# Optimization experiments

Hardware: AMD Instinct MI355X
Metric: run time of the kernel (lower is better)

Reference implementation:

```python
import jax, jax.numpy as jnp
import numpy as np

N = 100000
E = 1600000
H = 128
G = 64  # num graphs


def setup_inputs() -> dict:
    key = jax.random.key(0)
    ks = jax.random.split(key, 20)
    s = 1.0 / np.sqrt(H)
    inp = {
        'x': jax.random.normal(ks[0], (N,), jnp.float32),
        'edge_index': jax.random.randint(ks[1], (2, E), 0, N, jnp.int32),
        'edge_attr': jax.random.normal(ks[2], (E, 1), jnp.float32),
        'batch': jnp.sort(jax.random.randint(ks[3], (N,), 0, G, jnp.int32)),
        # node/edge encoders (Linear(1, H))
        'ne_w': jax.random.normal(ks[4], (1, H), jnp.float32),
        'ne_b': jnp.zeros((H,), jnp.float32),
        'ee_w': jax.random.normal(ks[5], (1, H), jnp.float32),
        'ee_b': jnp.zeros((H,), jnp.float32),
        # conv1: internal edge lin (Linear(H,H)) + MLP (H->H->H)
        'lin1_w': jax.random.normal(ks[6], (H, H), jnp.float32) * s,
        'lin1_b': jnp.zeros((H,), jnp.float32),
        'w11': jax.random.normal(ks[7], (H, H), jnp.float32) * s,
        'b11': jnp.zeros((H,), jnp.float32),
        'w12': jax.random.normal(ks[8], (H, H), jnp.float32) * s,
        'b12': jnp.zeros((H,), jnp.float32),
        # conv2
        'lin2_w': jax.random.normal(ks[9], (H, H), jnp.float32) * s,
        'lin2_b': jnp.zeros((H,), jnp.float32),
        'w21': jax.random.normal(ks[10], (H, H), jnp.float32) * s,
        'b21': jnp.zeros((H,), jnp.float32),
        'w22': jax.random.normal(ks[11], (H, H), jnp.float32) * s,
        'b22': jnp.zeros((H,), jnp.float32),
    }
    return inp


def _gine(h, edge_index, e, lin_w, lin_b, w1, b1, w2, b2, eps=0.0):
    # message: ReLU(x_j + Lin(edge_attr)), aggregated (sum) at target nodes
    src, dst = edge_index[0], edge_index[1]
    m = jax.nn.relu(h[src] + e @ lin_w + lin_b)           # [E, H]
    agg = jax.ops.segment_sum(m, dst, num_segments=N)      # [N, H]
    z = (1.0 + eps) * h + agg
    return jax.nn.relu(z @ w1 + b1) @ w2 + b2


def reference(x, edge_index, edge_attr, batch, ne_w, ne_b, ee_w, ee_b,
              lin1_w, lin1_b, w11, b11, w12, b12,
              lin2_w, lin2_b, w21, b21, w22, b22):
    h = x.reshape(-1, 1) @ ne_w + ne_b                     # [N, H]
    e = edge_attr @ ee_w + ee_b                            # [E, H]
    h = jax.nn.relu(_gine(h, edge_index, e, lin1_w, lin1_b, w11, b11, w12, b12))
    h = jax.nn.relu(_gine(h, edge_index, e, lin2_w, lin2_b, w21, b21, w22, b22))
    # global mean pool per graph
    sums = jax.ops.segment_sum(h, batch, num_segments=G)   # [G, H]
    cnt = jax.ops.segment_sum(jnp.ones((N,), h.dtype), batch, num_segments=G)
    return sums / jnp.maximum(cnt, 1.0)[:, None]
```

## Files before the change

### kernel.cpp

```cpp
#include <hip/hip_runtime.h>

typedef unsigned short u16;
typedef unsigned int u32;
typedef __bf16 bfrag __attribute__((ext_vector_type(8)));
typedef float f32x4 __attribute__((ext_vector_type(4)));
typedef float f32x2 __attribute__((ext_vector_type(2)));

__device__ __forceinline__ u16 f2bf(float f) {
    u32 u = __float_as_uint(f);
    u32 r = (u + 0x7FFFu + ((u >> 16) & 1u)) >> 16;
    return (u16)r;
}
__device__ __forceinline__ float bf2f(u32 h) {
    return __uint_as_float(h << 16);
}

__global__ __launch_bounds__(256) void prepack_consts_kernel(
    const float* __restrict__ w11, const float* __restrict__ w12,
    const float* __restrict__ w21, const float* __restrict__ w22,
    u16* __restrict__ hi, u16* __restrict__ lo,
    const float* __restrict__ ne_b, const float* __restrict__ ee_w, const float* __restrict__ ee_b,
    const float* __restrict__ lin1_w, const float* __restrict__ lin1_b,
    const float* __restrict__ lin2_w, const float* __restrict__ lin2_b,
    float* __restrict__ u1, float* __restrict__ C1, float* __restrict__ u2, float* __restrict__ C2)
{
    if (blockIdx.x == 256) {
        int c = threadIdx.x;
        if (c < 128) {
            float s1 = 0.f, t1 = 0.f, s2 = 0.f, t2 = 0.f;
            for (int k = 0; k < 128; ++k) {
                float w1 = lin1_w[k * 128 + c];
                float w2 = lin2_w[k * 128 + c];
                float ew = ee_w[k], eb = ee_b[k];
                s1 = fmaf(ew, w1, s1); t1 = fmaf(eb, w1, t1);
                s2 = fmaf(ew, w2, s2); t2 = fmaf(eb, w2, t2);
            }
            u1[c] = s1; C1[c] = t1 + lin1_b[c] + ne_b[c];
            u2[c] = s2; C2[c] = t2 + lin2_b[c];
        }
        return;
    }
    int which = blockIdx.x >> 6;
    const float* w = (which == 0) ? w11 : (which == 1) ? w12 : (which == 2) ? w21 : w22;
    int o = (blockIdx.x & 63) * 256 + threadIdx.x;
    int j = o & 7;
    int lane = (o >> 3) & 63;
    int ct = (o >> 9) & 7;
    int ks = o >> 12;
    int k = ks * 32 + ((lane >> 4) * 8) + j;
    int c = ct * 16 + (lane & 15);
    float v = w[k * 128 + c];
    u16 h = f2bf(v);
    float vh = bf2f(h);
    u16 l = f2bf(v - vh);
    hi[which * 16384 + o] = h;
    lo[which * 16384 + o] = l;
}

__global__ __launch_bounds__(1024) void bcount_kernel(
    const int* __restrict__ dst, int* __restrict__ bcnt, int* __restrict__ done,
    int* __restrict__ bstart, int* __restrict__ bcur, int E, int nb)
{
    __shared__ int h[256];
    __shared__ int is_last;
    if (threadIdx.x < 256) h[threadIdx.x] = 0;
    __syncthreads();
    int idx = blockIdx.x * 1024 + threadIdx.x;
    int e = idx * 4;
    if (e + 3 < E) {
        int4 d4 = ((const int4*)dst)[idx];
        atomicAdd(&h[d4.x >> 9], 1);
        atomicAdd(&h[d4.y >> 9], 1);
        atomicAdd(&h[d4.z >> 9], 1);
        atomicAdd(&h[d4.w >> 9], 1);
    } else {
        for (int k = e; k < E; ++k) atomicAdd(&h[dst[k] >> 9], 1);
    }
    __syncthreads();
    if (threadIdx.x < 256 && h[threadIdx.x]) atomicAdd(&bcnt[threadIdx.x], h[threadIdx.x]);
    __syncthreads();
    if (threadIdx.x == 0) {
        __threadfence();
        is_last = (atomicAdd(done, 1) == (int)gridDim.x - 1);
    }
    __syncthreads();
    if (!is_last) return;
    if (threadIdx.x < 256) h[threadIdx.x] = atomicAdd(&bcnt[threadIdx.x], 0);
    __syncthreads();
    __shared__ int excl[256];
    if (threadIdx.x < 64) {
        int l = threadIdx.x;
        int v0 = h[4 * l], v1 = h[4 * l + 1], v2 = h[4 * l + 2], v3 = h[4 * l + 3];
        int tot = v0 + v1 + v2 + v3;
        int run = tot;
#pragma unroll
        for (int off = 1; off < 64; off <<= 1) {
            int t = __shfl_up(run, off);
            if (l >= off) run += t;
        }
        int ex = run - tot;
        excl[4 * l] = ex;
        excl[4 * l + 1] = ex + v0;
        excl[4 * l + 2] = ex + v0 + v1;
        excl[4 * l + 3] = ex + v0 + v1 + v2;
    }
    __syncthreads();
    if (threadIdx.x < nb) {
        int ex = excl[threadIdx.x];
        bstart[threadIdx.x] = ex;
        bcur[threadIdx.x] = ex;
        if (threadIdx.x == nb - 1) bstart[nb] = ex + h[threadIdx.x];
    }
}

__global__ __launch_bounds__(1024) void bin_kernel(
    const int* __restrict__ src, const int* __restrict__ dst, const float* __restrict__ eattr,
    int* __restrict__ bucket_cursor,
    int2* __restrict__ binned, int E, int nb)
{
    __shared__ int hist[256];
    __shared__ int basel[256];
    __shared__ int gbase[256];
    __shared__ int2 stage[4096];
    __shared__ unsigned char sb[4096];
    const int tid = threadIdx.x;
    const int e0 = blockIdx.x * 4096;
    const int valid = min(4096, E - e0);

    if (tid < 256) hist[tid] = 0;
    __syncthreads();

    int d[4], s[4], a[4], rk[4];
    bool ok[4];
    const int eb = e0 + tid * 4;
    if (eb + 3 < E) {
        int4 d4 = *(const int4*)(dst + eb);
        int4 s4 = *(const int4*)(src + eb);
        int4 a4 = *(const int4*)((const int*)eattr + eb);
        d[0] = d4.x; d[1] = d4.y; d[2] = d4.z; d[3] = d4.w;
        s[0] = s4.x; s[1] = s4.y; s[2] = s4.z; s[3] = s4.w;
        a[0] = a4.x; a[1] = a4.y; a[2] = a4.z; a[3] = a4.w;
        ok[0] = ok[1] = ok[2] = ok[3] = true;
    } else {
#pragma unroll
        for (int k = 0; k < 4; ++k) {
            int e = eb + k;
            ok[k] = e < E;
            if (ok[k]) {
                d[k] = dst[e];
                s[k] = src[e];
                a[k] = __float_as_int(eattr[e]);
            }
        }
    }
#pragma unroll
    for (int k = 0; k < 4; ++k) {
        if (ok[k]) rk[k] = atomicAdd(&hist[d[k] >> 9], 1);
    }
    __syncthreads();
    if (tid < 64) {
        int l = tid;
        int v0 = hist[4 * l], v1 = hist[4 * l + 1], v2 = hist[4 * l + 2], v3 = hist[4 * l + 3];
        int tot = v0 + v1 + v2 + v3;
        int run = tot;
#pragma unroll
        for (int off = 1; off < 64; off <<= 1) {
            int t = __shfl_up(run, off);
            if (l >= off) run += t;
        }
        int ex = run - tot;
        basel[4 * l] = ex;
        basel[4 * l + 1] = ex + v0;
        basel[4 * l + 2] = ex + v0 + v1;
        basel[4 * l + 3] = ex + v0 + v1 + v2;
    }
    __syncthreads();
    if (tid < nb && hist[tid] > 0) gbase[tid] = atomicAdd(&bucket_cursor[tid], hist[tid]);
#pragma unroll
    for (int k = 0; k < 4; ++k) {
        if (ok[k]) {
            int b = d[k] >> 9;
            int pos = basel[b] + rk[k];
            stage[pos] = make_int2(s[k] | ((d[k] & 511) << 17), a[k]);
            sb[pos] = (unsigned char)b;
        }
    }
    __syncthreads();
    for (int i = tid; i < valid; i += 1024) {
        int b = (int)sb[i];
        binned[gbase[b] + (i - basel[b])] = stage[i];
    }
}

__global__ __launch_bounds__(1024) void fine_kernel(
    const int2* __restrict__ binned, const int* __restrict__ bstart,
    int* __restrict__ rowptr, int2* __restrict__ edges, int N, int nbuckets)
{
    __shared__ int hist[512];
    __shared__ int excl[512];
    const int tid = threadIdx.x;
    const int b = blockIdx.x;
    const int s0 = bstart[b], s1 = bstart[b + 1];
    if (tid < 512) hist[tid] = 0;
    __syncthreads();
    for (int i = s0 + tid; i < s1; i += 1024)
        atomicAdd(&hist[(binned[i].x >> 17) & 511], 1);
    __syncthreads();
    if (tid < 64) {
        int l = tid;
        int v[8], pre[8];
        int tot = 0;
#pragma unroll
        for (int k = 0; k < 8; ++k) { v[k] = hist[8 * l + k]; pre[k] = tot; tot += v[k]; }
        int run = tot;
#pragma unroll
        for (int off = 1; off < 64; off <<= 1) {
            int t = __shfl_up(run, off);
            if (l >= off) run += t;
        }
        int ex = run - tot;
#pragma unroll
        for (int k = 0; k < 8; ++k) excl[8 * l + k] = ex + pre[k];
    }
    __syncthreads();
    const int nbase = b << 9;
    if (tid < 512 && nbase + tid < N) rowptr[nbase + tid] = s0 + excl[tid];
    if (b == nbuckets - 1 && tid == 0) rowptr[N] = s1;
    __syncthreads();
    for (int i = s0 + tid; i < s1; i += 1024) {
        int2 ed = binned[i];
        int dlo = (ed.x >> 17) & 511;
        ed.x &= 0x1FFFF;
        int pos = atomicAdd(&excl[dlo], 1);
        edges[s0 + pos] = ed;
    }
}


__global__ __launch_bounds__(256) void pull1_kernel(
    const float* __restrict__ x,
    const int* __restrict__ rowptr, const int2* __restrict__ edges,
    const float* __restrict__ ne_w, const float* __restrict__ ne_b,
    const float* __restrict__ u1, const float* __restrict__ C1,
    u16* __restrict__ zb, int N)
{
    int lane = threadIdx.x & 63;
    int node = blockIdx.x * 4 + (threadIdx.x >> 6);
    if (node >= N) return;
    f32x2 A  = *(const f32x2*)(ne_w + 2 * lane);
    f32x2 Bv = *(const f32x2*)(u1   + 2 * lane);
    f32x2 Cv = *(const f32x2*)(C1   + 2 * lane);
    f32x2 nb = *(const f32x2*)(ne_b + 2 * lane);
    const f32x2 zero = {0.f, 0.f};
    int jb = rowptr[node], je = rowptr[node + 1];
    f32x2 acc = zero;
    int j = jb;
    for (; j + 8 <= je; j += 8) {
        float xs[8], av[8];
#pragma unroll
        for (int t = 0; t < 8; ++t) {
            int2 ep = edges[j + t];
            int s = __builtin_amdgcn_readfirstlane(ep.x);
            av[t] = __int_as_float(__builtin_amdgcn_readfirstlane(ep.y));
            xs[t] = x[s];
        }
#pragma unroll
        for (int t = 0; t < 8; ++t) {
            f32x2 m = __builtin_elementwise_fma((f32x2){xs[t], xs[t]}, A,
                        __builtin_elementwise_fma((f32x2){av[t], av[t]}, Bv, Cv));
            acc += __builtin_elementwise_max(m, zero);
        }
    }
    for (; j < je; ++j) {
        int2 ep = edges[j];
        int s = __builtin_amdgcn_readfirstlane(ep.x);
        float av = __int_as_float(__builtin_amdgcn_readfirstlane(ep.y));
        float xs = x[s];
        f32x2 m = __builtin_elementwise_fma((f32x2){xs, xs}, A,
                    __builtin_elementwise_fma((f32x2){av, av}, Bv, Cv));
        acc += __builtin_elementwise_max(m, zero);
    }
    float xn = x[node];
    f32x2 z = __builtin_elementwise_fma((f32x2){xn, xn}, A, nb) + acc;
    ((u32*)(zb + (long)node * 128))[lane] = (u32)f2bf(z.x) | ((u32)f2bf(z.y) << 16);
}

__global__ __launch_bounds__(256) void pull2_kernel(
    const u16* __restrict__ h1b,
    const int* __restrict__ rowptr, const int2* __restrict__ edges,
    const float* __restrict__ u2, const float* __restrict__ C2,
    u16* __restrict__ zb2, int N)
{
    int lane = threadIdx.x & 63;
    int node = blockIdx.x * 4 + (threadIdx.x >> 6);
    if (node >= N) return;
    f32x2 Bv = *(const f32x2*)(u2 + 2 * lane);
    f32x2 Cv = *(const f32x2*)(C2 + 2 * lane);
    const f32x2 zero = {0.f, 0.f};
    int jb = rowptr[node], je = rowptr[node + 1];
    f32x2 acc = zero;
    int j = jb;
    for (; j + 8 <= je; j += 8) {
        int sidx[8];
        float av[8];
        u32 hv[8];
#pragma unroll
        for (int t = 0; t < 8; ++t) {
            int2 ep = edges[j + t];
            sidx[t] = __builtin_amdgcn_readfirstlane(ep.x);
            av[t] = __int_as_float(__builtin_amdgcn_readfirstlane(ep.y));
        }
#pragma unroll
        for (int t = 0; t < 8; ++t)
            hv[t] = *(const u32*)(h1b + (long)sidx[t] * 128 + 2 * lane);
#pragma unroll
        for (int t = 0; t < 8; ++t) {
            f32x2 h = { __uint_as_float(hv[t] << 16), __uint_as_float(hv[t] & 0xFFFF0000u) };
            f32x2 m = h + __builtin_elementwise_fma((f32x2){av[t], av[t]}, Bv, Cv);
            acc += __builtin_elementwise_max(m, zero);
        }
    }
    for (; j < je; ++j) {
        int2 ep = edges[j];
        int s = __builtin_amdgcn_readfirstlane(ep.x);
        float av = __int_as_float(__builtin_amdgcn_readfirstlane(ep.y));
        u32 hv = *(const u32*)(h1b + (long)s * 128 + 2 * lane);
        f32x2 h = { __uint_as_float(hv << 16), __uint_as_float(hv & 0xFFFF0000u) };
        f32x2 m = h + __builtin_elementwise_fma((f32x2){av, av}, Bv, Cv);
        acc += __builtin_elementwise_max(m, zero);
    }
    u32 hn = *(const u32*)(h1b + (long)node * 128 + 2 * lane);
    f32x2 hnv = { __uint_as_float(hn << 16), __uint_as_float(hn & 0xFFFF0000u) };
    f32x2 z = hnv + acc;
    ((u32*)(zb2 + (long)node * 128))[lane] = (u32)f2bf(z.x) | ((u32)f2bf(z.y) << 16);
}

__global__ __launch_bounds__(256) void mlp_kernel(
    const u16* __restrict__ zb,
    const u16* __restrict__ w1hi, const u16* __restrict__ w1lo,
    const u16* __restrict__ w2hi, const u16* __restrict__ w2lo,
    const float* __restrict__ b1, const float* __restrict__ b2,
    u16* __restrict__ outb)
{
    __shared__ __align__(16) u16 tls[64][136];
    const int lane = threadIdx.x & 63;
    const int wv = threadIdx.x >> 6;
    const int m = lane & 15;
    const int q = lane >> 4;
    const int ko = q * 8;
    const long tile_row = (long)blockIdx.x * 64 + wv * 16;

    f32x4 acc[8];
#pragma unroll
    for (int ct = 0; ct < 8; ++ct) acc[ct] = (f32x4){0.f, 0.f, 0.f, 0.f};

#pragma unroll
    for (int ks = 0; ks < 4; ++ks) {
        bfrag a = *(const bfrag*)(zb + (tile_row + m) * 128 + ks * 32 + ko);
#pragma unroll
        for (int ct = 0; ct < 8; ++ct) {
            const int off = (((ks * 8 + ct) * 64) + lane) * 8;
            bfrag bh = *(const bfrag*)(w1hi + off);
            bfrag bl = *(const bfrag*)(w1lo + off);
            acc[ct] = __builtin_amdgcn_mfma_f32_16x16x32_bf16(a, bh, acc[ct], 0, 0, 0);
            acc[ct] = __builtin_amdgcn_mfma_f32_16x16x32_bf16(a, bl, acc[ct], 0, 0, 0);
        }
    }
#pragma unroll
    for (int ct = 0; ct < 8; ++ct) {
        float bv = b1[ct * 16 + m];
#pragma unroll
        for (int r = 0; r < 4; ++r) {
            float v = fmaxf(acc[ct][r] + bv, 0.f);
            tls[wv * 16 + q * 4 + r][ct * 16 + m] = f2bf(v);
        }
    }
    __syncthreads();

    f32x4 acc2[8];
#pragma unroll
    for (int ct = 0; ct < 8; ++ct) acc2[ct] = (f32x4){0.f, 0.f, 0.f, 0.f};

#pragma unroll
    for (int ks = 0; ks < 4; ++ks) {
        bfrag a = *(const bfrag*)(&tls[wv * 16 + m][ks * 32 + ko]);
#pragma unroll
        for (int ct = 0; ct < 8; ++ct) {
            const int off = (((ks * 8 + ct) * 64) + lane) * 8;
            bfrag bh = *(const bfrag*)(w2hi + off);
            bfrag bl = *(const bfrag*)(w2lo + off);
            acc2[ct] = __builtin_amdgcn_mfma_f32_16x16x32_bf16(a, bh, acc2[ct], 0, 0, 0);
            acc2[ct] = __builtin_amdgcn_mfma_f32_16x16x32_bf16(a, bl, acc2[ct], 0, 0, 0);
        }
    }
    __syncthreads();
#pragma unroll
    for (int ct = 0; ct < 8; ++ct) {
        float bv = b2[ct * 16 + m];
#pragma unroll
        for (int r = 0; r < 4; ++r) {
            float v = fmaxf(acc2[ct][r] + bv, 0.f);
            tls[wv * 16 + q * 4 + r][ct * 16 + m] = f2bf(v);
        }
    }
    __syncthreads();
    const long base_row = (long)blockIdx.x * 64;
#pragma unroll
    for (int it = 0; it < 4; ++it) {
        int chunk = threadIdx.x + it * 256;
        int row = chunk >> 4;
        int c8 = (chunk & 15) * 8;
        *(uint4*)(outb + (base_row + row) * 128 + c8) = *(const uint4*)(&tls[row][c8]);
    }
}

__global__ __launch_bounds__(256) void mlp_pool_kernel(
    const u16* __restrict__ zb,
    const u16* __restrict__ w1hi, const u16* __restrict__ w1lo,
    const u16* __restrict__ w2hi, const u16* __restrict__ w2lo,
    const float* __restrict__ b1, const float* __restrict__ b2,
    const int* __restrict__ batch, float* __restrict__ poolacc, int N)
{
    __shared__ __align__(16) u16 tls[64][136];
    __shared__ int bsh[64];
    const int lane = threadIdx.x & 63;
    const int wv = threadIdx.x >> 6;
    const int m = lane & 15;
    const int q = lane >> 4;
    const int ko = q * 8;
    const long tile_row = (long)blockIdx.x * 64 + wv * 16;
    const long base_row = (long)blockIdx.x * 64;

    if (threadIdx.x < 64) {
        long node = base_row + threadIdx.x;
        bsh[threadIdx.x] = (node < N) ? batch[node] : -1;
    }

    f32x4 acc[8];
#pragma unroll
    for (int ct = 0; ct < 8; ++ct) acc[ct] = (f32x4){0.f, 0.f, 0.f, 0.f};

#pragma unroll
    for (int ks = 0; ks < 4; ++ks) {
        bfrag a = *(const bfrag*)(zb + (tile_row + m) * 128 + ks * 32 + ko);
#pragma unroll
        for (int ct = 0; ct < 8; ++ct) {
            const int off = (((ks * 8 + ct) * 64) + lane) * 8;
            bfrag bh = *(const bfrag*)(w1hi + off);
            bfrag bl = *(const bfrag*)(w1lo + off);
            acc[ct] = __builtin_amdgcn_mfma_f32_16x16x32_bf16(a, bh, acc[ct], 0, 0, 0);
            acc[ct] = __builtin_amdgcn_mfma_f32_16x16x32_bf16(a, bl, acc[ct], 0, 0, 0);
        }
    }
#pragma unroll
    for (int ct = 0; ct < 8; ++ct) {
        float bv = b1[ct * 16 + m];
#pragma unroll
        for (int r = 0; r < 4; ++r) {
            float v = fmaxf(acc[ct][r] + bv, 0.f);
            tls[wv * 16 + q * 4 + r][ct * 16 + m] = f2bf(v);
        }
    }
    __syncthreads();

    f32x4 acc2[8];
#pragma unroll
    for (int ct = 0; ct < 8; ++ct) acc2[ct] = (f32x4){0.f, 0.f, 0.f, 0.f};

#pragma unroll
    for (int ks = 0; ks < 4; ++ks) {
        bfrag a = *(const bfrag*)(&tls[wv * 16 + m][ks * 32 + ko]);
#pragma unroll
        for (int ct = 0; ct < 8; ++ct) {
            const int off = (((ks * 8 + ct) * 64) + lane) * 8;
            bfrag bh = *(const bfrag*)(w2hi + off);
            bfrag bl = *(const bfrag*)(w2lo + off);
            acc2[ct] = __builtin_amdgcn_mfma_f32_16x16x32_bf16(a, bh, acc2[ct], 0, 0, 0);
            acc2[ct] = __builtin_amdgcn_mfma_f32_16x16x32_bf16(a, bl, acc2[ct], 0, 0, 0);
        }
    }
    __syncthreads();
#pragma unroll
    for (int ct = 0; ct < 8; ++ct) {
        float bv = b2[ct * 16 + m];
#pragma unroll
        for (int r = 0; r < 4; ++r) {
            float v = fmaxf(acc2[ct][r] + bv, 0.f);
            tls[wv * 16 + q * 4 + r][ct * 16 + m] = f2bf(v);
        }
    }
    __syncthreads();

    int c = threadIdx.x & 127;
    int half = threadIdx.x >> 7;
    int r0 = half * 32, r1 = r0 + 32;
    int cur = -1;
    float sum = 0.f;
    for (int r = r0; r < r1; ++r) {
        int g = bsh[r];
        if (g < 0) break;
        float v = bf2f((u32)tls[r][c]);
        if (g != cur) {
            if (cur >= 0) atomicAdd(&poolacc[cur * 128 + c], sum);
            sum = 0.f;
            cur = g;
        }
        sum += v;
    }
    if (cur >= 0) atomicAdd(&poolacc[cur * 128 + c], sum);
}

__global__ __launch_bounds__(128) void pool2_kernel(
    const float* __restrict__ acc, const int* __restrict__ batch,
    float* __restrict__ out, int n)
{
    int g = blockIdx.x;
    int c = threadIdx.x;
    int lo = 0, hi = n;
    while (lo < hi) { int mid = (lo + hi) >> 1; if (batch[mid] < g) lo = mid + 1; else hi = mid; }
    int s = lo;
    lo = s; hi = n;
    while (lo < hi) { int mid = (lo + hi) >> 1; if (batch[mid] < g + 1) lo = mid + 1; else hi = mid; }
    int cnt = lo - s;
    out[g * 128 + c] = acc[g * 128 + c] / (float)(cnt > 0 ? cnt : 1);
}

extern "C" void kernel_launch(void* const* d_in, const int* in_sizes, int n_in,
                              void* d_out, int out_size, void* d_ws, size_t ws_size,
                              hipStream_t stream)
{
    const float* x      = (const float*)d_in[0];
    const int*   ei     = (const int*)d_in[1];
    const float* eattr  = (const float*)d_in[2];
    const int*   batch  = (const int*)d_in[3];
    const float* ne_w   = (const float*)d_in[4];
    const float* ne_b   = (const float*)d_in[5];
    const float* ee_w   = (const float*)d_in[6];
    const float* ee_b   = (const float*)d_in[7];
    const float* lin1_w = (const float*)d_in[8];
    const float* lin1_b = (const float*)d_in[9];
    const float* w11    = (const float*)d_in[10];
    const float* b11    = (const float*)d_in[11];
    const float* w12    = (const float*)d_in[12];
    const float* b12    = (const float*)d_in[13];
    const float* lin2_w = (const float*)d_in[14];
    const float* lin2_b = (const float*)d_in[15];
    const float* w21    = (const float*)d_in[16];
    const float* b21    = (const float*)d_in[17];
    const float* w22    = (const float*)d_in[18];
    const float* b22    = (const float*)d_in[19];

    const int N = in_sizes[0];
    const int E = in_sizes[2];
    const int G = out_size / 128;
    const int Npad = ((N + 63) / 64) * 64;
    const int nb = (N + 511) >> 9;
    const int* esrc = ei;
    const int* edst = ei + E;

    char* p = (char*)d_ws;
    auto alloc = [&](size_t bytes) -> void* {
        void* r = (void*)p;
        p += (bytes + 255) & ~(size_t)255;
        return r;
    };
    float* u1 = (float*)alloc(128 * 4);
    float* C1 = (float*)alloc(128 * 4);
    float* u2 = (float*)alloc(128 * 4);
    float* C2 = (float*)alloc(128 * 4);
    int* bcnt   = (int*)alloc(1024);
    int* done   = (int*)alloc(256);
    float* poolacc = (float*)alloc((size_t)G * 128 * 4);
    int* bstart = (int*)alloc(((size_t)nb + 1) * 4);
    int* bcur   = (int*)alloc((size_t)nb * 4);
    int* rowptr = (int*)alloc(((size_t)N + 1) * 4);
    int2* edges = (int2*)alloc((size_t)E * 8);
    int2* binned = (int2*)alloc((size_t)E * 8);
    u16* whi = (u16*)alloc((size_t)4 * 16384 * 2);
    u16* wlo = (u16*)alloc((size_t)4 * 16384 * 2);
    u16* bufA = (u16*)alloc((size_t)Npad * 128 * 2);
    u16* bufB = (u16*)alloc((size_t)Npad * 128 * 2);

    size_t zbytes = (size_t)((char*)poolacc + (size_t)G * 128 * 4 - (char*)bcnt);
    hipMemsetAsync(bcnt, 0, zbytes, stream);

    prepack_consts_kernel<<<257, 256, 0, stream>>>(
        w11, w12, w21, w22, whi, wlo,
        ne_b, ee_w, ee_b, lin1_w, lin1_b, lin2_w, lin2_b, u1, C1, u2, C2);

    bcount_kernel<<<(E + 4095) / 4096, 1024, 0, stream>>>(edst, bcnt, done, bstart, bcur, E, nb);
    bin_kernel<<<(E + 4095) / 4096, 1024, 0, stream>>>(esrc, edst, eattr, bcur, binned, E, nb);
    fine_kernel<<<nb, 1024, 0, stream>>>(binned, bstart, rowptr, edges, N, nb);

    pull1_kernel<<<(N + 3) / 4, 256, 0, stream>>>(x, rowptr, edges, ne_w, ne_b, u1, C1,
                                                  bufA, N);
    mlp_kernel<<<Npad / 64, 256, 0, stream>>>(bufA, whi, wlo, whi + 16384, wlo + 16384,
                                              b11, b12, bufB);
    pull2_kernel<<<(N + 3) / 4, 256, 0, stream>>>(bufB, rowptr, edges, u2, C2, bufA, N);
    mlp_pool_kernel<<<Npad / 64, 256, 0, stream>>>(bufA, whi + 32768, wlo + 32768,
                                                   whi + 49152, wlo + 49152, b21, b22,
                                                   batch, poolacc, N);

    pool2_kernel<<<G, 128, 0, stream>>>(poolacc, batch, (float*)d_out, N);
}
```

Baseline: 362.9 us.

## Fuse neighbor aggregation into MLP kernels via shared-memory tiles

Merges each layer's pull (gather and sum over incoming edges) into the following MLP kernel. Each wave aggregates its 16 nodes directly into the shared tile that feeds the MFMA matmuls. This removes the global write and read of the bf16 aggregated features and two kernel launches, and it drops __syncthreads that are redundant because each wave only touches its own rows. The trade-off is fewer, larger blocks with each wave processing 16 nodes serially. That may reduce latency hiding for the irregular gathers and raise register pressure.

```diff
diff --git a/kernel.cpp b/kernel.cpp
--- a/kernel.cpp
+++ b/kernel.cpp
@@ -236,119 +236,69 @@
     }
 }
 
-
-__global__ __launch_bounds__(256) void pull1_kernel(
+__global__ __launch_bounds__(256) void fused1_kernel(
     const float* __restrict__ x,
     const int* __restrict__ rowptr, const int2* __restrict__ edges,
     const float* __restrict__ ne_w, const float* __restrict__ ne_b,
     const float* __restrict__ u1, const float* __restrict__ C1,
-    u16* __restrict__ zb, int N)
-{
-    int lane = threadIdx.x & 63;
-    int node = blockIdx.x * 4 + (threadIdx.x >> 6);
-    if (node >= N) return;
-    f32x2 A  = *(const f32x2*)(ne_w + 2 * lane);
-    f32x2 Bv = *(const f32x2*)(u1   + 2 * lane);
-    f32x2 Cv = *(const f32x2*)(C1   + 2 * lane);
-    f32x2 nb = *(const f32x2*)(ne_b + 2 * lane);
-    const f32x2 zero = {0.f, 0.f};
-    int jb = rowptr[node], je = rowptr[node + 1];
-    f32x2 acc = zero;
-    int j = jb;
-    for (; j + 8 <= je; j += 8) {
-        float xs[8], av[8];
-#pragma unroll
-        for (int t = 0; t < 8; ++t) {
-            int2 ep = edges[j + t];
-            int s = __builtin_amdgcn_readfirstlane(ep.x);
-            av[t] = __int_as_float(__builtin_amdgcn_readfirstlane(ep.y));
-            xs[t] = x[s];
-        }
-#pragma unroll
-        for (int t = 0; t < 8; ++t) {
-            f32x2 m = __builtin_elementwise_fma((f32x2){xs[t], xs[t]}, A,
-                        __builtin_elementwise_fma((f32x2){av[t], av[t]}, Bv, Cv));
-            acc += __builtin_elementwise_max(m, zero);
-        }
-    }
-    for (; j < je; ++j) {
-        int2 ep = edges[j];
-        int s = __builtin_amdgcn_readfirstlane(ep.x);
-        float av = __int_as_float(__builtin_amdgcn_readfirstlane(ep.y));
-        float xs = x[s];
-        f32x2 m = __builtin_elementwise_fma((f32x2){xs, xs}, A,
-                    __builtin_elementwise_fma((f32x2){av, av}, Bv, Cv));
-        acc += __builtin_elementwise_max(m, zero);
-    }
-    float xn = x[node];
-    f32x2 z = __builtin_elementwise_fma((f32x2){xn, xn}, A, nb) + acc;
-    ((u32*)(zb + (long)node * 128))[lane] = (u32)f2bf(z.x) | ((u32)f2bf(z.y) << 16);
-}
-
-__global__ __launch_bounds__(256) void pull2_kernel(
-    const u16* __restrict__ h1b,
-    const int* __restrict__ rowptr, const int2* __restrict__ edges,
-    const float* __restrict__ u2, const float* __restrict__ C2,
-    u16* __restrict__ zb2, int N)
-{
-    int lane = threadIdx.x & 63;
-    int node = blockIdx.x * 4 + (threadIdx.x >> 6);
-    if (node >= N) return;
-    f32x2 Bv = *(const f32x2*)(u2 + 2 * lane);
-    f32x2 Cv = *(const f32x2*)(C2 + 2 * lane);
-    const f32x2 zero = {0.f, 0.f};
-    int jb = rowptr[node], je = rowptr[node + 1];
-    f32x2 acc = zero;
-    int j = jb;
-    for (; j + 8 <= je; j += 8) {
-        int sidx[8];
-        float av[8];
-        u32 hv[8];
-#pragma unroll
-        for (int t = 0; t < 8; ++t) {
-            int2 ep = edges[j + t];
-            sidx[t] = __builtin_amdgcn_readfirstlane(ep.x);
-            av[t] = __int_as_float(__builtin_amdgcn_readfirstlane(ep.y));
-        }
-#pragma unroll
-        for (int t = 0; t < 8; ++t)
-            hv[t] = *(const u32*)(h1b + (long)sidx[t] * 128 + 2 * lane);
-#pragma unroll
-        for (int t = 0; t < 8; ++t) {
-            f32x2 h = { __uint_as_float(hv[t] << 16), __uint_as_float(hv[t] & 0xFFFF0000u) };
-            f32x2 m = h + __builtin_elementwise_fma((f32x2){av[t], av[t]}, Bv, Cv);
-            acc += __builtin_elementwise_max(m, zero);
-        }
-    }
-    for (; j < je; ++j) {
-        int2 ep = edges[j];
-        int s = __builtin_amdgcn_readfirstlane(ep.x);
-        float av = __int_as_float(__builtin_amdgcn_readfirstlane(ep.y));
-        u32 hv = *(const u32*)(h1b + (long)s * 128 + 2 * lane);
-        f32x2 h = { __uint_as_float(hv << 16), __uint_as_float(hv & 0xFFFF0000u) };
-        f32x2 m = h + __builtin_elementwise_fma((f32x2){av, av}, Bv, Cv);
-        acc += __builtin_elementwise_max(m, zero);
-    }
-    u32 hn = *(const u32*)(h1b + (long)node * 128 + 2 * lane);
-    f32x2 hnv = { __uint_as_float(hn << 16), __uint_as_float(hn & 0xFFFF0000u) };
-    f32x2 z = hnv + acc;
-    ((u32*)(zb2 + (long)node * 128))[lane] = (u32)f2bf(z.x) | ((u32)f2bf(z.y) << 16);
-}
-
-__global__ __launch_bounds__(256) void mlp_kernel(
-    const u16* __restrict__ zb,
     const u16* __restrict__ w1hi, const u16* __restrict__ w1lo,
     const u16* __restrict__ w2hi, const u16* __restrict__ w2lo,
     const float* __restrict__ b1, const float* __restrict__ b2,
-    u16* __restrict__ outb)
+    u16* __restrict__ outb, int N)
 {
     __shared__ __align__(16) u16 tls[64][136];
     const int lane = threadIdx.x & 63;
     const int wv = threadIdx.x >> 6;
+    const long base_row = (long)blockIdx.x * 64;
+
+    f32x2 A   = *(const f32x2*)(ne_w + 2 * lane);
+    f32x2 Bv  = *(const f32x2*)(u1   + 2 * lane);
+    f32x2 Cv  = *(const f32x2*)(C1   + 2 * lane);
+    f32x2 nbv = *(const f32x2*)(ne_b + 2 * lane);
+    const f32x2 zero = {0.f, 0.f};
+
+    for (int i = 0; i < 16; ++i) {
+        const int node = (int)base_row + wv * 16 + i;
+        f32x2 z = zero;
+        if (node < N) {
+            const int jb = __builtin_amdgcn_readfirstlane(rowptr[node]);
+            const int je = __builtin_amdgcn_readfirstlane(rowptr[node + 1]);
+            f32x2 acc = zero;
+            int j = jb;
+            for (; j + 8 <= je; j += 8) {
+                float xs[8], av[8];
+#pragma unroll
+                for (int t = 0; t < 8; ++t) {
+                    int2 ep = edges[j + t];
+                    int s = __builtin_amdgcn_readfirstlane(ep.x);
+                    av[t] = __int_as_float(__builtin_amdgcn_readfirstlane(ep.y));
+                    xs[t] = x[s];
+                }
+#pragma unroll
+                for (int t = 0; t < 8; ++t) {
+                    f32x2 m = __builtin_elementwise_fma((f32x2){xs[t], xs[t]}, A,
+                                __builtin_elementwise_fma((f32x2){av[t], av[t]}, Bv, Cv));
+                    acc += __builtin_elementwise_max(m, zero);
+                }
+            }
+            for (; j < je; ++j) {
+                int2 ep = edges[j];
+                int s = __builtin_amdgcn_readfirstlane(ep.x);
+                float av = __int_as_float(__builtin_amdgcn_readfirstlane(ep.y));
+                float xs = x[s];
+                f32x2 m = __builtin_elementwise_fma((f32x2){xs, xs}, A,
+                            __builtin_elementwise_fma((f32x2){av, av}, Bv, Cv));
+                acc += __builtin_elementwise_max(m, zero);
+            }
+            float xn = x[node];
+            z = __builtin_elementwise_fma((f32x2){xn, xn}, A, nbv) + acc;
+        }
+        ((u32*)&tls[wv * 16 + i][0])[lane] = (u32)f2bf(z.x) | ((u32)f2bf(z.y) << 16);
+    }
+
     const int m = lane & 15;
     const int q = lane >> 4;
     const int ko = q * 8;
-    const long tile_row = (long)blockIdx.x * 64 + wv * 16;
 
     f32x4 acc[8];
 #pragma unroll
@@ -356,7 +306,7 @@
 
 #pragma unroll
     for (int ks = 0; ks < 4; ++ks) {
-        bfrag a = *(const bfrag*)(zb + (tile_row + m) * 128 + ks * 32 + ko);
+        bfrag a = *(const bfrag*)(&tls[wv * 16 + m][ks * 32 + ko]);
 #pragma unroll
         for (int ct = 0; ct < 8; ++ct) {
             const int off = (((ks * 8 + ct) * 64) + lane) * 8;
@@ -375,7 +325,6 @@
             tls[wv * 16 + q * 4 + r][ct * 16 + m] = f2bf(v);
         }
     }
-    __syncthreads();
 
     f32x4 acc2[8];
 #pragma unroll
@@ -393,7 +342,6 @@
             acc2[ct] = __builtin_amdgcn_mfma_f32_16x16x32_bf16(a, bl, acc2[ct], 0, 0, 0);
         }
     }
-    __syncthreads();
 #pragma unroll
     for (int ct = 0; ct < 8; ++ct) {
         float bv = b2[ct * 16 + m];
@@ -404,7 +352,6 @@
         }
     }
     __syncthreads();
-    const long base_row = (long)blockIdx.x * 64;
 #pragma unroll
     for (int it = 0; it < 4; ++it) {
         int chunk = threadIdx.x + it * 256;
@@ -414,8 +361,10 @@
     }
 }
 
-__global__ __launch_bounds__(256) void mlp_pool_kernel(
-    const u16* __restrict__ zb,
+__global__ __launch_bounds__(256) void fused2_kernel(
+    const u16* __restrict__ h1b,
+    const int* __restrict__ rowptr, const int2* __restrict__ edges,
+    const float* __restrict__ u2, const float* __restrict__ C2,
     const u16* __restrict__ w1hi, const u16* __restrict__ w1lo,
     const u16* __restrict__ w2hi, const u16* __restrict__ w2lo,
     const float* __restrict__ b1, const float* __restrict__ b2,
@@ -425,16 +374,64 @@
     __shared__ int bsh[64];
     const int lane = threadIdx.x & 63;
     const int wv = threadIdx.x >> 6;
+    const long base_row = (long)blockIdx.x * 64;
+
+    if (threadIdx.x < 64) {
+        long node = base_row + threadIdx.x;
+        bsh[threadIdx.x] = (node < N) ? batch[node] : -1;
+    }
+
+    f32x2 Bv = *(const f32x2*)(u2 + 2 * lane);
+    f32x2 Cv = *(const f32x2*)(C2 + 2 * lane);
+    const f32x2 zero = {0.f, 0.f};
+
+    for (int i = 0; i < 16; ++i) {
+        const int node = (int)base_row + wv * 16 + i;
+        f32x2 z = zero;
+        if (node < N) {
+            const int jb = __builtin_amdgcn_readfirstlane(rowptr[node]);
+            const int je = __builtin_amdgcn_readfirstlane(rowptr[node + 1]);
+            f32x2 acc = zero;
+            int j = jb;
+            for (; j + 8 <= je; j += 8) {
+                int sidx[8];
+                float av[8];
+                u32 hv[8];
+#pragma unroll
+                for (int t = 0; t < 8; ++t) {
+                    int2 ep = edges[j + t];
+                    sidx[t] = __builtin_amdgcn_readfirstlane(ep.x);
+                    av[t] = __int_as_float(__builtin_amdgcn_readfirstlane(ep.y));
+                }
+#pragma unroll
+                for (int t = 0; t < 8; ++t)
+                    hv[t] = *(const u32*)(h1b + (long)sidx[t] * 128 + 2 * lane);
+#pragma unroll
+                for (int t = 0; t < 8; ++t) {
+                    f32x2 h = { __uint_as_float(hv[t] << 16), __uint_as_float(hv[t] & 0xFFFF0000u) };
+                    f32x2 m = h + __builtin_elementwise_fma((f32x2){av[t], av[t]}, Bv, Cv);
+                    acc += __builtin_elementwise_max(m, zero);
+                }
+            }
+            for (; j < je; ++j) {
+                int2 ep = edges[j];
+                int s = __builtin_amdgcn_readfirstlane(ep.x);
+                float av = __int_as_float(__builtin_amdgcn_readfirstlane(ep.y));
+                u32 hv = *(const u32*)(h1b + (long)s * 128 + 2 * lane);
+                f32x2 h = { __uint_as_float(hv << 16), __uint_as_float(hv & 0xFFFF0000u) };
+                f32x2 m = h + __builtin_elementwise_fma((f32x2){av, av}, Bv, Cv);
+                acc += __builtin_elementwise_max(m, zero);
+            }
+            u32 hn = *(const u32*)(h1b + (long)node * 128 + 2 * lane);
+            f32x2 hnv = { __uint_as_float(hn << 16), __uint_as_float(hn & 0xFFFF0000u) };
+            z = hnv + acc;
+        }
+        ((u32*)&tls[wv * 16 + i][0])[lane] = (u32)f2bf(z.x) | ((u32)f2bf(z.y) << 16);
+    }
+
     const int m = lane & 15;
     const int q = lane >> 4;
     const int ko = q * 8;
-    const long tile_row = (long)blockIdx.x * 64 + wv * 16;
-    const long base_row = (long)blockIdx.x * 64;
-
-    if (threadIdx.x < 64) {
-        long node = base_row + threadIdx.x;
-        bsh[threadIdx.x] = (node < N) ? batch[node] : -1;
-    }
 
     f32x4 acc[8];
 #pragma unroll
@@ -442,7 +439,7 @@
 
 #pragma unroll
     for (int ks = 0; ks < 4; ++ks) {
-        bfrag a = *(const bfrag*)(zb + (tile_row + m) * 128 + ks * 32 + ko);
+        bfrag a = *(const bfrag*)(&tls[wv * 16 + m][ks * 32 + ko]);
 #pragma unroll
         for (int ct = 0; ct < 8; ++ct) {
             const int off = (((ks * 8 + ct) * 64) + lane) * 8;
@@ -461,7 +458,6 @@
             tls[wv * 16 + q * 4 + r][ct * 16 + m] = f2bf(v);
         }
     }
-    __syncthreads();
 
     f32x4 acc2[8];
 #pragma unroll
@@ -479,7 +475,6 @@
             acc2[ct] = __builtin_amdgcn_mfma_f32_16x16x32_bf16(a, bl, acc2[ct], 0, 0, 0);
         }
     }
-    __syncthreads();
 #pragma unroll
     for (int ct = 0; ct < 8; ++ct) {
         float bv = b2[ct * 16 + m];
@@ -578,7 +573,6 @@
     int2* binned = (int2*)alloc((size_t)E * 8);
     u16* whi = (u16*)alloc((size_t)4 * 16384 * 2);
     u16* wlo = (u16*)alloc((size_t)4 * 16384 * 2);
-    u16* bufA = (u16*)alloc((size_t)Npad * 128 * 2);
     u16* bufB = (u16*)alloc((size_t)Npad * 128 * 2);
 
     size_t zbytes = (size_t)((char*)poolacc + (size_t)G * 128 * 4 - (char*)bcnt);
@@ -592,14 +586,13 @@
     bin_kernel<<<(E + 4095) / 4096, 1024, 0, stream>>>(esrc, edst, eattr, bcur, binned, E, nb);
     fine_kernel<<<nb, 1024, 0, stream>>>(binned, bstart, rowptr, edges, N, nb);
 
-    pull1_kernel<<<(N + 3) / 4, 256, 0, stream>>>(x, rowptr, edges, ne_w, ne_b, u1, C1,
-                                                  bufA, N);
-    mlp_kernel<<<Npad / 64, 256, 0, stream>>>(bufA, whi, wlo, whi + 16384, wlo + 16384,
-                                              b11, b12, bufB);
-    pull2_kernel<<<(N + 3) / 4, 256, 0, stream>>>(bufB, rowptr, edges, u2, C2, bufA, N);
-    mlp_pool_kernel<<<Npad / 64, 256, 0, stream>>>(bufA, whi + 32768, wlo + 32768,
-                                                   whi + 49152, wlo + 49152, b21, b22,
-                                                   batch, poolacc, N);
+    fused1_kernel<<<Npad / 64, 256, 0, stream>>>(
+        x, rowptr, edges, ne_w, ne_b, u1, C1,
+        whi, wlo, whi + 16384, wlo + 16384, b11, b12, bufB, N);
+    fused2_kernel<<<Npad / 64, 256, 0, stream>>>(
+        bufB, rowptr, edges, u2, C2,
+        whi + 32768, wlo + 32768, whi + 49152, wlo + 49152, b21, b22,
+        batch, poolacc, N);
 
     pool2_kernel<<<G, 128, 0, stream>>>(poolacc, batch, (float*)d_out, N);
 }
```

Result: slower. 444.4 us (+22.5%).
